# Performance work log

Hardware: AMD Instinct MI355X
Metric: run time of the kernel (lower is better)

The kernel has to match this reference:

```python
import jax, jax.numpy as jnp
import numpy as np

B, S, D_MODEL, H = 2, 2048, 1024, 16
DK = D_MODEL // H
THETA = 10000.0


def setup_inputs() -> dict:
    key = jax.random.key(0)
    ks = jax.random.split(key, 5)
    scale = 0.02  # keep logits in a numerically sane range
    return {
        "x": jax.random.normal(ks[0], (B, S, D_MODEL), jnp.float32),
        "Q_weight": jax.random.normal(ks[1], (D_MODEL, D_MODEL), jnp.float32) * scale,
        "K_weight": jax.random.normal(ks[2], (D_MODEL, D_MODEL), jnp.float32) * scale,
        "V_weight": jax.random.normal(ks[3], (D_MODEL, D_MODEL), jnp.float32) * scale,
        "O_weight": jax.random.normal(ks[4], (D_MODEL, D_MODEL), jnp.float32) * scale,
        "token_positions": jnp.arange(S, dtype=jnp.int32),
    }


def _rope(x, token_positions, theta, d_k):
    # x: [..., seq, d_k]; rotate interleaved even/odd pairs
    inv_freq = 1.0 / theta ** (jnp.arange(0, d_k, 2, dtype=jnp.float32) / d_k)
    ang = token_positions.astype(jnp.float32)[:, None] * inv_freq  # [S, d_k/2]
    cos, sin = jnp.cos(ang), jnp.sin(ang)
    x0, x1 = x[..., 0::2], x[..., 1::2]
    y0 = x0 * cos - x1 * sin
    y1 = x0 * sin + x1 * cos
    return jnp.stack([y0, y1], axis=-1).reshape(x.shape)


def _mhsa(x, Qw, Kw, Vw, Ow, token_positions):
    b, s, d = x.shape
    qw = Qw.reshape(H, DK, d)
    kw = Kw.reshape(H, DK, d)
    vw = Vw.reshape(H, DK, d)
    q = jnp.einsum('hki,bsi->bhsk', qw, x)
    k = jnp.einsum('hki,bsi->bhsk', kw, x)
    v = jnp.einsum('hvi,bsi->bhsv', vw, x)
    q = _rope(q, token_positions, THETA, DK)
    k = _rope(k, token_positions, THETA, DK)
    scores = jnp.einsum('bhnd,bhmd->bhnm', q, k) / jnp.sqrt(jnp.float32(DK))
    causal = jnp.tril(jnp.ones((s, s), dtype=bool))
    scores = jnp.where(causal, scores, -jnp.inf)
    attn = jax.nn.softmax(scores, axis=-1)
    o = jnp.einsum('bhnm,bhmv->bhnv', attn, v)  # [B,H,S,DV]
    o = jnp.transpose(o, (0, 2, 1, 3)).reshape(b, s, H * DK)
    return jnp.einsum('dv,bsv->bsd', Ow, o)


def reference(x, Q_weight, K_weight, V_weight, O_weight, token_positions):
    return _mhsa(x, Q_weight, K_weight, V_weight, O_weight, token_positions)
```

## Files before the change

kernel.cpp:

```cpp
#include <hip/hip_runtime.h>

#define NB 2
#define NS 2048
#define NDM 1024
#define NH 16
#define NDK 64

typedef unsigned int u32;
typedef u32 u32x4 __attribute__((ext_vector_type(4)));
typedef float f32x4 __attribute__((ext_vector_type(4)));
typedef float f32x2 __attribute__((ext_vector_type(2)));
typedef __bf16 bf16x8 __attribute__((ext_vector_type(8)));
typedef __bf16 bf16x4 __attribute__((ext_vector_type(4)));
typedef __bf16 bf16x2 __attribute__((ext_vector_type(2)));

#define QSCALE 0.18033688011112042f
#define EXP2F(x) __builtin_amdgcn_exp2f(x)

__device__ __forceinline__ void gload_lds16(const __bf16* g, __bf16* l) {
    __builtin_amdgcn_global_load_lds(
        (const __attribute__((address_space(1))) unsigned int*)(g),
        (__attribute__((address_space(3))) unsigned int*)(l), 16, 0, 0);
}

__global__ __launch_bounds__(256) void cvt_all(const float* __restrict__ x,
                                               const float* __restrict__ qw,
                                               const float* __restrict__ kw,
                                               const float* __restrict__ vw,
                                               const float* __restrict__ ow,
                                               __bf16* __restrict__ xb,
                                               __bf16* __restrict__ wqkv,
                                               __bf16* __restrict__ owb) {
    const int i = blockIdx.x * 256 + threadIdx.x;
    const float* src;
    __bf16* dst;
    if (i < 1048576) {
        src = x + (size_t)i * 4;
        dst = xb + (size_t)i * 4;
    } else {
        const int j = i - 1048576;
        const int seg = j >> 18;
        const int off = j & 0x3FFFF;
        src = ((seg == 0) ? qw : (seg == 1) ? kw : (seg == 2) ? vw : ow) + (size_t)off * 4;
        dst = ((seg == 3) ? owb : wqkv + (size_t)seg * 1048576) + (size_t)off * 4;
    }
    f32x4 v = *(const f32x4*)src;
    bf16x4 o;
    o[0] = (__bf16)v[0]; o[1] = (__bf16)v[1]; o[2] = (__bf16)v[2]; o[3] = (__bf16)v[3];
    *(bf16x4*)dst = o;
}

__global__ __launch_bounds__(256) void rope_table(const int* __restrict__ tp,
                                                  float* __restrict__ tbl) {
    const int i = blockIdx.x * 256 + threadIdx.x;
    if (i >= NS * 32) return;
    const int s = i >> 5, jj = i & 31;
    const float pos = (float)tp[s];
    const float inv = exp2f(-0.41524101186092f * (float)jj);
    const float ang = pos * inv;
    float sn, cs;
    sincosf(ang, &sn, &cs);
    f32x2 o; o[0] = cs; o[1] = sn;
    *(f32x2*)&tbl[(size_t)i * 2] = o;
}

__global__ __launch_bounds__(512, 2) void gemm256(const __bf16* __restrict__ A,
                                                  const __bf16* __restrict__ Bt,
                                                  __bf16* __restrict__ C,
                                                  __bf16* __restrict__ Vt,
                                                  int K, int lda, int ldb, int ldc, int nbx) {
    __shared__ __bf16 As[2][256 * 64];
    __shared__ __bf16 Bs[2][256 * 64];
    const int tid = threadIdx.x;
    const int lane = tid & 63, w = tid >> 6;
    const int wm = w >> 2, wn = w & 3;
    const int l15 = lane & 15, lg = lane >> 4;
    int bid = blockIdx.x;
    const int cpx = gridDim.x >> 3;
    bid = (bid & 7) * cpx + (bid >> 3);
    const int m0 = (bid / nbx) * 256, n0 = (bid % nbx) * 256;
    const int srow = w * 8 + (lane >> 3);
    const int csw = ((lane & 7) ^ (srow & 7)) * 8;

    f32x4 acc[8][4];
    const f32x4 z = {0.f, 0.f, 0.f, 0.f};
#pragma unroll
    for (int i = 0; i < 8; ++i)
#pragma unroll
        for (int jx = 0; jx < 4; ++jx) acc[i][jx] = z;

    auto stage_pass = [&](int buf, int k0, int ps) {
        const int r = ps * 64 + srow;
        gload_lds16(&A[(size_t)(m0 + r) * lda + k0 + csw], &As[buf][(ps * 64 + w * 8) * 64]);
        gload_lds16(&Bt[(size_t)(n0 + r) * ldb + k0 + csw], &Bs[buf][(ps * 64 + w * 8) * 64]);
    };

#pragma unroll
    for (int ps = 0; ps < 4; ++ps) stage_pass(0, 0, ps);
    int cur = 0;
    for (int k0 = 0; k0 < K; k0 += 64) {
        const bool hasnext = (k0 + 64 < K);
        asm volatile("s_waitcnt vmcnt(0)" ::: "memory");
        __builtin_amdgcn_s_barrier();
        __builtin_amdgcn_sched_barrier(0);
        bf16x8 bfr[4][2];
#pragma unroll
        for (int ph = 0; ph < 4; ++ph) {
            if (ph == 0) {
#pragma unroll
                for (int n = 0; n < 4; ++n)
#pragma unroll
                    for (int kc = 0; kc < 2; ++kc) {
                        const int rb = wn * 64 + n * 16 + l15;
                        bfr[n][kc] = *(const bf16x8*)&Bs[cur][rb * 64 + ((kc * 32 + lg * 8) ^ ((rb & 7) << 3))];
                    }
            }
            bf16x8 a0[2], a1[2];
#pragma unroll
            for (int kc = 0; kc < 2; ++kc) {
                const int ra0 = wm * 128 + (2 * ph) * 16 + l15;
                const int ra1 = wm * 128 + (2 * ph + 1) * 16 + l15;
                a0[kc] = *(const bf16x8*)&As[cur][ra0 * 64 + ((kc * 32 + lg * 8) ^ ((ra0 & 7) << 3))];
                a1[kc] = *(const bf16x8*)&As[cur][ra1 * 64 + ((kc * 32 + lg * 8) ^ ((ra1 & 7) << 3))];
            }
            if (hasnext) stage_pass(cur ^ 1, k0 + 64, ph);
            __builtin_amdgcn_s_barrier();
            asm volatile("s_waitcnt lgkmcnt(0)" ::: "memory");
            __builtin_amdgcn_sched_barrier(0);
            __builtin_amdgcn_s_setprio(1);
#pragma unroll
            for (int n = 0; n < 4; ++n)
#pragma unroll
                for (int kc = 0; kc < 2; ++kc) {
                    acc[2 * ph][n]     = __builtin_amdgcn_mfma_f32_16x16x32_bf16(a0[kc], bfr[n][kc], acc[2 * ph][n], 0, 0, 0);
                    acc[2 * ph + 1][n] = __builtin_amdgcn_mfma_f32_16x16x32_bf16(a1[kc], bfr[n][kc], acc[2 * ph + 1][n], 0, 0, 0);
                }
            __builtin_amdgcn_s_setprio(0);
            __builtin_amdgcn_s_barrier();
            __builtin_amdgcn_sched_barrier(0);
        }
        cur ^= 1;
    }
    if (n0 < 2048) {
#pragma unroll
        for (int mr = 0; mr < 8; ++mr)
#pragma unroll
            for (int n = 0; n < 4; ++n)
#pragma unroll
                for (int j = 0; j < 4; ++j) {
                    const int row = m0 + wm * 128 + mr * 16 + lg * 4 + j;
                    const int col = n0 + wn * 64 + n * 16 + l15;
                    C[(size_t)row * ldc + col] = (__bf16)acc[mr][n][j];
                }
    } else {
#pragma unroll
        for (int mr = 0; mr < 8; ++mr)
#pragma unroll
            for (int n = 0; n < 4; ++n) {
                const int col = (n0 - 2048) + wn * 64 + n * 16 + l15;
                const int h = col >> 6, d = col & 63;
                const int row = m0 + wm * 128 + mr * 16 + lg * 4;
                const int b = row >> 11, s = row & (NS - 1);
                bf16x4 ov;
#pragma unroll
                for (int j = 0; j < 4; ++j) ov[j] = (__bf16)acc[mr][n][j];
                *(bf16x4*)&Vt[((size_t)(b * NH + h) * 64 + d) * NS + s] = ov;
            }
    }
}

template <typename TOUT>
__global__ __launch_bounds__(256) void gemm_bt128(const __bf16* __restrict__ A,
                                                  const __bf16* __restrict__ Bt,
                                                  TOUT* __restrict__ C,
                                                  int K, int lda, int ldb, int ldc) {
    __shared__ __bf16 As[2][128 * 64];
    __shared__ __bf16 Bs[2][128 * 64];
    const int tid = threadIdx.x;
    const int lane = tid & 63, w = tid >> 6;
    const int wr = w >> 1, wc = w & 1;
    const int l15 = lane & 15, lg = lane >> 4;
    const int m0 = blockIdx.y * 128, n0 = blockIdx.x * 128;
    const int crow = lane >> 3;
    const int csw = ((lane & 7) ^ crow) * 8;

    f32x4 acc[4][4];
    const f32x4 z = {0.f, 0.f, 0.f, 0.f};
#pragma unroll
    for (int i = 0; i < 4; ++i)
#pragma unroll
        for (int jx = 0; jx < 4; ++jx) acc[i][jx] = z;

    auto stage = [&](int buf, int k0) {
#pragma unroll
        for (int ch = 0; ch < 4; ++ch) {
            const int cid = w * 4 + ch;
            const int ra = cid * 8 + crow;
            gload_lds16(&A[(size_t)(m0 + ra) * lda + k0 + csw], &As[buf][cid * 512]);
            gload_lds16(&Bt[(size_t)(n0 + ra) * ldb + k0 + csw], &Bs[buf][cid * 512]);
        }
    };

    stage(0, 0);
    int cur = 0;
    for (int k0 = 0; k0 < K; k0 += 64) {
        if (k0 + 64 < K) {
            stage(cur ^ 1, k0 + 64);
            asm volatile("s_waitcnt vmcnt(8)" ::: "memory");
        } else {
            asm volatile("s_waitcnt vmcnt(0)" ::: "memory");
        }
        __builtin_amdgcn_s_barrier();
        __builtin_amdgcn_sched_barrier(0);
#pragma unroll
        for (int kc = 0; kc < 2; ++kc) {
            bf16x8 af[4], bfv[4];
#pragma unroll
            for (int i = 0; i < 4; ++i) {
                const int ra = wr * 64 + i * 16 + l15;
                const int rb = wc * 64 + i * 16 + l15;
                af[i]  = *(const bf16x8*)&As[cur][ra * 64 + ((kc * 32 + lg * 8) ^ ((ra & 7) << 3))];
                bfv[i] = *(const bf16x8*)&Bs[cur][rb * 64 + ((kc * 32 + lg * 8) ^ ((rb & 7) << 3))];
            }
#pragma unroll
            for (int sm = 0; sm < 4; ++sm)
#pragma unroll
                for (int sn = 0; sn < 4; ++sn)
                    acc[sm][sn] = __builtin_amdgcn_mfma_f32_16x16x32_bf16(af[sm], bfv[sn], acc[sm][sn], 0, 0, 0);
        }
        asm volatile("s_waitcnt lgkmcnt(0)" ::: "memory");
        __builtin_amdgcn_s_barrier();
        __builtin_amdgcn_sched_barrier(0);
        cur ^= 1;
    }
#pragma unroll
    for (int sm = 0; sm < 4; ++sm)
#pragma unroll
        for (int sn = 0; sn < 4; ++sn)
#pragma unroll
            for (int j = 0; j < 4; ++j) {
                const int row = m0 + wr * 64 + sm * 16 + lg * 4 + j;
                const int col = n0 + wc * 64 + sn * 16 + l15;
                C[(size_t)row * ldc + col] = (TOUT)acc[sm][sn][j];
            }
}

__global__ __launch_bounds__(512) void rope_kernel(const __bf16* __restrict__ qkv,
                                                   const float* __restrict__ tbl,
                                                   __bf16* __restrict__ Qr,
                                                   __bf16* __restrict__ Kr) {
    const int row = blockIdx.x;
    const int s = row & (NS - 1);
    const int b = row >> 11;
    const int t = threadIdx.x;
    const int h = t >> 5, jj = t & 31;
    f32x2 cssn = *(const f32x2*)&tbl[((size_t)s * 32 + jj) * 2];
    const float cs = cssn[0], sn = cssn[1];
    const __bf16* qp = qkv + (size_t)row * 3072 + h * 64 + 2 * jj;
    bf16x2 qv = *(const bf16x2*)qp;
    bf16x2 kv = *(const bf16x2*)(qp + 1024);
    const float q0 = (float)qv[0], q1 = (float)qv[1];
    const float k0 = (float)kv[0], k1 = (float)kv[1];
    const size_t o = ((size_t)(b * NH + h) * NS + s) * 64 + 2 * jj;
    bf16x2 qo, ko;
    qo[0] = (__bf16)((q0 * cs - q1 * sn) * QSCALE);
    qo[1] = (__bf16)((q0 * sn + q1 * cs) * QSCALE);
    ko[0] = (__bf16)(k0 * cs - k1 * sn); ko[1] = (__bf16)(k0 * sn + k1 * cs);
    *(bf16x2*)&Qr[o] = qo;
    *(bf16x2*)&Kr[o] = ko;
}

__device__ __forceinline__ int kperm(int rt) {
    const int ct = rt >> 4, rr = rt & 15;
    return ((rr >> 2) << 3) + ((ct >> 1) << 5) + ((ct & 1) << 2) + (rr & 3);
}

__global__ __launch_bounds__(256) void attn5(const __bf16* __restrict__ Qr,
                                             const __bf16* __restrict__ Kr,
                                             const __bf16* __restrict__ Vt,
                                             __bf16* __restrict__ O) {
    const int lid = blockIdx.x;
    const int xcd = lid & 7;
    const int g = lid >> 3;
    const int bh = xcd * 4 + (g & 3);
    const int pr = g >> 2;
    const int p = (pr < 8) ? (pr * 2) : (31 - 2 * pr);
    const int b = bh >> 4, h = bh & 15;
    const int tid = threadIdx.x;
    const int w = tid >> 6, lane = tid & 63;
    const int l15 = lane & 15, lg = lane >> 4;
    const __bf16* Qb = Qr + (size_t)bh * NS * 64;
    const __bf16* Kb = Kr + (size_t)bh * NS * 64;
    const __bf16* Vb = Vt + (size_t)bh * 64 * NS;

    __shared__ __bf16 Ks[2][64 * 64];
    __shared__ __bf16 Vs[2][64 * 64];

    const int rbv[2] = {p * 64 + w * 16, (31 - p) * 64 + w * 16};

    bf16x8 qf[2][2];
#pragma unroll
    for (int rs = 0; rs < 2; ++rs)
#pragma unroll
        for (int kc = 0; kc < 2; ++kc)
            qf[rs][kc] = *(const bf16x8*)(Qb + (size_t)(rbv[rs] + l15) * 64 + kc * 32 + lg * 8);

    f32x4 oacc[2][4];
    const f32x4 z = {0.f, 0.f, 0.f, 0.f};
#pragma unroll
    for (int rs = 0; rs < 2; ++rs)
#pragma unroll
        for (int ct = 0; ct < 4; ++ct) oacc[rs][ct] = z;
    float lsum[2] = {0.f, 0.f};

    const int crow = lane >> 3;
    const int cswz = ((lane & 7) ^ crow) * 8;

#pragma unroll
    for (int pp = 0; pp < 2; ++pp) {
        const int ch = w + pp * 4;
        const int rt = ch * 8 + crow;
        gload_lds16(Kb + (size_t)kperm(rt) * 64 + cswz, &Ks[0][ch * 512]);
        gload_lds16(Vb + (size_t)rt * NS + 0 + cswz, &Vs[0][ch * 512]);
    }
    __syncthreads();

    const int nt = 32 - p;
    for (int t = 0; t < nt; ++t) {
        const int cur = t & 1;
        const int kv0 = t << 6;
        if (t + 1 < nt) {
            const int kv1 = kv0 + 64;
#pragma unroll
            for (int pp = 0; pp < 2; ++pp) {
                const int ch = w + pp * 4;
                const int rt = ch * 8 + crow;
                gload_lds16(Kb + (size_t)(kv1 + kperm(rt)) * 64 + cswz, &Ks[cur ^ 1][ch * 512]);
                gload_lds16(Vb + (size_t)rt * NS + kv1 + cswz, &Vs[cur ^ 1][ch * 512]);
            }
        }
        bool act[2];
        act[0] = (kv0 <= rbv[0] + 15);
        act[1] = true;
        f32x4 sc[2][4];
#pragma unroll
        for (int rs = 0; rs < 2; ++rs)
            if (act[rs])
#pragma unroll
                for (int ct = 0; ct < 4; ++ct) sc[rs][ct] = z;
#pragma unroll
        for (int kc = 0; kc < 2; ++kc) {
            bf16x8 kf[4];
#pragma unroll
            for (int ct = 0; ct < 4; ++ct) {
                const int rt = ct * 16 + l15;
                kf[ct] = *(const bf16x8*)&Ks[cur][rt * 64 + ((kc * 32 + lg * 8) ^ ((rt & 7) << 3))];
            }
#pragma unroll
            for (int rs = 0; rs < 2; ++rs)
                if (act[rs])
#pragma unroll
                    for (int ct = 0; ct < 4; ++ct)
                        sc[rs][ct] = __builtin_amdgcn_mfma_f32_16x16x32_bf16(kf[ct], qf[rs][kc], sc[rs][ct], 0, 0, 0);
        }
        bf16x8 pb[2][2];
#pragma unroll
        for (int rs = 0; rs < 2; ++rs) {
            if (!act[rs]) continue;
            const int rbase = rbv[rs];
            const int qrow = rbase + l15;
            const bool needmask = (kv0 + 63 > rbase);
            if (needmask) {
#pragma unroll
                for (int ct = 0; ct < 4; ++ct)
#pragma unroll
                    for (int j = 0; j < 4; ++j) {
                        const int kvg = kv0 + ((ct >> 1) << 5) + lg * 8 + ((ct & 1) << 2) + j;
                        if (kvg > qrow) sc[rs][ct][j] = -1e30f;
                    }
            }
            float ps = 0.f;
#pragma unroll
            for (int ct = 0; ct < 4; ++ct)
#pragma unroll
                for (int j = 0; j < 4; ++j) {
                    const float e = EXP2F(sc[rs][ct][j]);
                    sc[rs][ct][j] = e;
                    ps += e;
                }
            ps += __shfl_xor(ps, 16, 64);
            ps += __shfl_xor(ps, 32, 64);
            lsum[rs] += ps;
#pragma unroll
            for (int kc = 0; kc < 2; ++kc) {
                bf16x8 pk;
                pk[0] = (__bf16)sc[rs][2 * kc][0];     pk[1] = (__bf16)sc[rs][2 * kc][1];
                pk[2] = (__bf16)sc[rs][2 * kc][2];     pk[3] = (__bf16)sc[rs][2 * kc][3];
                pk[4] = (__bf16)sc[rs][2 * kc + 1][0]; pk[5] = (__bf16)sc[rs][2 * kc + 1][1];
                pk[6] = (__bf16)sc[rs][2 * kc + 1][2]; pk[7] = (__bf16)sc[rs][2 * kc + 1][3];
                pb[rs][kc] = pk;
            }
        }
#pragma unroll
        for (int kc = 0; kc < 2; ++kc) {
            bf16x8 vf[4];
#pragma unroll
            for (int ct = 0; ct < 4; ++ct) {
                const int rt = ct * 16 + l15;
                vf[ct] = *(const bf16x8*)&Vs[cur][rt * 64 + ((kc * 32 + lg * 8) ^ ((rt & 7) << 3))];
            }
#pragma unroll
            for (int rs = 0; rs < 2; ++rs) {
                if (!act[rs]) continue;
#pragma unroll
                for (int ct = 0; ct < 4; ++ct)
                    oacc[rs][ct] = __builtin_amdgcn_mfma_f32_16x16x32_bf16(vf[ct], pb[rs][kc], oacc[rs][ct], 0, 0, 0);
            }
        }
        __syncthreads();
    }
#pragma unroll
    for (int rs = 0; rs < 2; ++rs) {
        const float rl = 1.0f / lsum[rs];
        const size_t rowoff = (size_t)(b * NS + rbv[rs] + l15) * NDM + h * 64 + lg * 4;
#pragma unroll
        for (int ct = 0; ct < 4; ++ct) {
            bf16x4 ov;
#pragma unroll
            for (int j = 0; j < 4; ++j) ov[j] = (__bf16)(oacc[rs][ct][j] * rl);
            *(bf16x4*)&O[rowoff + ct * 16] = ov;
        }
    }
}

extern "C" void kernel_launch(void* const* d_in, const int* in_sizes, int n_in,
                              void* d_out, int out_size, void* d_ws, size_t ws_size,
                              hipStream_t stream) {
    const float* x  = (const float*)d_in[0];
    const float* Qw = (const float*)d_in[1];
    const float* Kw = (const float*)d_in[2];
    const float* Vw = (const float*)d_in[3];
    const float* Ow = (const float*)d_in[4];
    const int*   tp = (const int*)d_in[5];
    float* out = (float*)d_out;

    char* ws = (char*)d_ws;
    size_t off = 0;
    auto alloc = [&](size_t bytes) -> void* {
        void* p = ws + off;
        off += (bytes + 255) & ~(size_t)255;
        return p;
    };
    __bf16* xb   = (__bf16*)alloc((size_t)4096 * 1024 * 2);
    __bf16* wqkv = (__bf16*)alloc((size_t)3072 * 1024 * 2);
    __bf16* owb  = (__bf16*)alloc((size_t)1024 * 1024 * 2);
    __bf16* qkv  = (__bf16*)alloc((size_t)4096 * 3072 * 2);
    __bf16* qr   = (__bf16*)alloc((size_t)32 * 2048 * 64 * 2);
    __bf16* kr   = (__bf16*)alloc((size_t)32 * 2048 * 64 * 2);
    __bf16* vt   = (__bf16*)alloc((size_t)32 * 64 * 2048 * 2);
    __bf16* ob   = (__bf16*)alloc((size_t)4096 * 1024 * 2);
    float*  tbl  = (float*)alloc((size_t)NS * 32 * 2 * 4);

    cvt_all<<<8192, 256, 0, stream>>>(x, Qw, Kw, Vw, Ow, xb, wqkv, owb);
    rope_table<<<(NS * 32 + 255) / 256, 256, 0, stream>>>(tp, tbl);

    gemm256<<<192, 512, 0, stream>>>(xb, wqkv, qkv, vt, 1024, 1024, 1024, 3072, 12);
    rope_kernel<<<4096, 512, 0, stream>>>(qkv, tbl, qr, kr);
    attn5<<<dim3(512), 256, 0, stream>>>(qr, kr, vt, ob);
    gemm_bt128<float><<<dim3(1024 / 128, 4096 / 128), 256, 0, stream>>>(
        ob, owb, out, 1024, 1024, 1024, 1024);
}
```

Measured before the change: 119.1 us.

## Use 128-tile QKV GEMM and 2-wave attention with 4 row strips per wave

Replaces the 256x256, 512-thread QKV projection GEMM with a 128x128, 256-thread kernel. The new kernel launches 768 blocks instead of 192, issues the next tile's loads before the MFMA loop, and waits with a partial vmcnt. The attention kernel drops from 4 waves to 2 waves per block, and each wave now owns four 16-row query strips instead of two. This is meant to improve CU fill for the GEMM and to reuse each K/V LDS fragment across more query rows. The cost is higher register pressure in attention and less B-operand reuse per block in the GEMM.

```diff
diff --git a/kernel.cpp b/kernel.cpp
--- a/kernel.cpp
+++ b/kernel.cpp
@@ -64,106 +64,93 @@
     *(f32x2*)&tbl[(size_t)i * 2] = o;
 }
 
-__global__ __launch_bounds__(512, 2) void gemm256(const __bf16* __restrict__ A,
-                                                  const __bf16* __restrict__ Bt,
-                                                  __bf16* __restrict__ C,
-                                                  __bf16* __restrict__ Vt,
-                                                  int K, int lda, int ldb, int ldc, int nbx) {
-    __shared__ __bf16 As[2][256 * 64];
-    __shared__ __bf16 Bs[2][256 * 64];
+__global__ __launch_bounds__(256) void gemm_qkv128(const __bf16* __restrict__ A,
+                                                   const __bf16* __restrict__ Bt,
+                                                   __bf16* __restrict__ C,
+                                                   __bf16* __restrict__ Vt) {
+    __shared__ __bf16 As[2][128 * 64];
+    __shared__ __bf16 Bs[2][128 * 64];
+    const int K = 1024, lda = 1024, ldb = 1024, ldc = 3072;
     const int tid = threadIdx.x;
     const int lane = tid & 63, w = tid >> 6;
-    const int wm = w >> 2, wn = w & 3;
+    const int wr = w >> 1, wc = w & 1;
     const int l15 = lane & 15, lg = lane >> 4;
-    int bid = blockIdx.x;
-    const int cpx = gridDim.x >> 3;
-    bid = (bid & 7) * cpx + (bid >> 3);
-    const int m0 = (bid / nbx) * 256, n0 = (bid % nbx) * 256;
-    const int srow = w * 8 + (lane >> 3);
-    const int csw = ((lane & 7) ^ (srow & 7)) * 8;
-
-    f32x4 acc[8][4];
+    const int m0 = blockIdx.y * 128, n0 = blockIdx.x * 128;
+    const int crow = lane >> 3;
+    const int csw = ((lane & 7) ^ crow) * 8;
+
+    f32x4 acc[4][4];
     const f32x4 z = {0.f, 0.f, 0.f, 0.f};
 #pragma unroll
-    for (int i = 0; i < 8; ++i)
+    for (int i = 0; i < 4; ++i)
 #pragma unroll
         for (int jx = 0; jx < 4; ++jx) acc[i][jx] = z;
 
-    auto stage_pass = [&](int buf, int k0, int ps) {
-        const int r = ps * 64 + srow;
-        gload_lds16(&A[(size_t)(m0 + r) * lda + k0 + csw], &As[buf][(ps * 64 + w * 8) * 64]);
-        gload_lds16(&Bt[(size_t)(n0 + r) * ldb + k0 + csw], &Bs[buf][(ps * 64 + w * 8) * 64]);
+    auto stage = [&](int buf, int k0) {
+#pragma unroll
+        for (int ch = 0; ch < 4; ++ch) {
+            const int cid = w * 4 + ch;
+            const int ra = cid * 8 + crow;
+            gload_lds16(&A[(size_t)(m0 + ra) * lda + k0 + csw], &As[buf][cid * 512]);
+            gload_lds16(&Bt[(size_t)(n0 + ra) * ldb + k0 + csw], &Bs[buf][cid * 512]);
+        }
     };
 
-#pragma unroll
-    for (int ps = 0; ps < 4; ++ps) stage_pass(0, 0, ps);
+    stage(0, 0);
     int cur = 0;
     for (int k0 = 0; k0 < K; k0 += 64) {
-        const bool hasnext = (k0 + 64 < K);
-        asm volatile("s_waitcnt vmcnt(0)" ::: "memory");
+        if (k0 + 64 < K) {
+            stage(cur ^ 1, k0 + 64);
+            asm volatile("s_waitcnt vmcnt(8)" ::: "memory");
+        } else {
+            asm volatile("s_waitcnt vmcnt(0)" ::: "memory");
+        }
         __builtin_amdgcn_s_barrier();
         __builtin_amdgcn_sched_barrier(0);
-        bf16x8 bfr[4][2];
-#pragma unroll
-        for (int ph = 0; ph < 4; ++ph) {
-            if (ph == 0) {
-#pragma unroll
-                for (int n = 0; n < 4; ++n)
-#pragma unroll
-                    for (int kc = 0; kc < 2; ++kc) {
-                        const int rb = wn * 64 + n * 16 + l15;
-                        bfr[n][kc] = *(const bf16x8*)&Bs[cur][rb * 64 + ((kc * 32 + lg * 8) ^ ((rb & 7) << 3))];
-                    }
-            }
-            bf16x8 a0[2], a1[2];
-#pragma unroll
-            for (int kc = 0; kc < 2; ++kc) {
-                const int ra0 = wm * 128 + (2 * ph) * 16 + l15;
-                const int ra1 = wm * 128 + (2 * ph + 1) * 16 + l15;
-                a0[kc] = *(const bf16x8*)&As[cur][ra0 * 64 + ((kc * 32 + lg * 8) ^ ((ra0 & 7) << 3))];
-                a1[kc] = *(const bf16x8*)&As[cur][ra1 * 64 + ((kc * 32 + lg * 8) ^ ((ra1 & 7) << 3))];
-            }
-            if (hasnext) stage_pass(cur ^ 1, k0 + 64, ph);
-            __builtin_amdgcn_s_barrier();
-            asm volatile("s_waitcnt lgkmcnt(0)" ::: "memory");
-            __builtin_amdgcn_sched_barrier(0);
-            __builtin_amdgcn_s_setprio(1);
-#pragma unroll
-            for (int n = 0; n < 4; ++n)
-#pragma unroll
-                for (int kc = 0; kc < 2; ++kc) {
-                    acc[2 * ph][n]     = __builtin_amdgcn_mfma_f32_16x16x32_bf16(a0[kc], bfr[n][kc], acc[2 * ph][n], 0, 0, 0);
-                    acc[2 * ph + 1][n] = __builtin_amdgcn_mfma_f32_16x16x32_bf16(a1[kc], bfr[n][kc], acc[2 * ph + 1][n], 0, 0, 0);
-                }
-            __builtin_amdgcn_s_setprio(0);
-            __builtin_amdgcn_s_barrier();
-            __builtin_amdgcn_sched_barrier(0);
-        }
+#pragma unroll
+        for (int kc = 0; kc < 2; ++kc) {
+            bf16x8 af[4], bfv[4];
+#pragma unroll
+            for (int i = 0; i < 4; ++i) {
+                const int ra = wr * 64 + i * 16 + l15;
+                const int rb = wc * 64 + i * 16 + l15;
+                af[i]  = *(const bf16x8*)&As[cur][ra * 64 + ((kc * 32 + lg * 8) ^ ((ra & 7) << 3))];
+                bfv[i] = *(const bf16x8*)&Bs[cur][rb * 64 + ((kc * 32 + lg * 8) ^ ((rb & 7) << 3))];
+            }
+#pragma unroll
+            for (int sm = 0; sm < 4; ++sm)
+#pragma unroll
+                for (int sn = 0; sn < 4; ++sn)
+                    acc[sm][sn] = __builtin_amdgcn_mfma_f32_16x16x32_bf16(af[sm], bfv[sn], acc[sm][sn], 0, 0, 0);
+        }
+        asm volatile("s_waitcnt lgkmcnt(0)" ::: "memory");
+        __builtin_amdgcn_s_barrier();
+        __builtin_amdgcn_sched_barrier(0);
         cur ^= 1;
     }
     if (n0 < 2048) {
 #pragma unroll
-        for (int mr = 0; mr < 8; ++mr)
-#pragma unroll
-            for (int n = 0; n < 4; ++n)
+        for (int sm = 0; sm < 4; ++sm)
+#pragma unroll
+            for (int sn = 0; sn < 4; ++sn)
 #pragma unroll
                 for (int j = 0; j < 4; ++j) {
-                    const int row = m0 + wm * 128 + mr * 16 + lg * 4 + j;
-                    const int col = n0 + wn * 64 + n * 16 + l15;
-                    C[(size_t)row * ldc + col] = (__bf16)acc[mr][n][j];
+                    const int row = m0 + wr * 64 + sm * 16 + lg * 4 + j;
+                    const int col = n0 + wc * 64 + sn * 16 + l15;
+                    C[(size_t)row * ldc + col] = (__bf16)acc[sm][sn][j];
                 }
     } else {
 #pragma unroll
-        for (int mr = 0; mr < 8; ++mr)
-#pragma unroll
-            for (int n = 0; n < 4; ++n) {
-                const int col = (n0 - 2048) + wn * 64 + n * 16 + l15;
+        for (int sm = 0; sm < 4; ++sm)
+#pragma unroll
+            for (int sn = 0; sn < 4; ++sn) {
+                const int col = (n0 - 2048) + wc * 64 + sn * 16 + l15;
                 const int h = col >> 6, d = col & 63;
-                const int row = m0 + wm * 128 + mr * 16 + lg * 4;
+                const int row = m0 + wr * 64 + sm * 16 + lg * 4;
                 const int b = row >> 11, s = row & (NS - 1);
                 bf16x4 ov;
 #pragma unroll
-                for (int j = 0; j < 4; ++j) ov[j] = (__bf16)acc[mr][n][j];
+                for (int j = 0; j < 4; ++j) ov[j] = (__bf16)acc[sm][sn][j];
                 *(bf16x4*)&Vt[((size_t)(b * NH + h) * 64 + d) * NS + s] = ov;
             }
     }
@@ -275,7 +262,7 @@
     return ((rr >> 2) << 3) + ((ct >> 1) << 5) + ((ct & 1) << 2) + (rr & 3);
 }
 
-__global__ __launch_bounds__(256) void attn5(const __bf16* __restrict__ Qr,
+__global__ __launch_bounds__(128) void attn7(const __bf16* __restrict__ Qr,
                                              const __bf16* __restrict__ Kr,
                                              const __bf16* __restrict__ Vt,
                                              __bf16* __restrict__ O) {
@@ -296,29 +283,30 @@
     __shared__ __bf16 Ks[2][64 * 64];
     __shared__ __bf16 Vs[2][64 * 64];
 
-    const int rbv[2] = {p * 64 + w * 16, (31 - p) * 64 + w * 16};
-
-    bf16x8 qf[2][2];
-#pragma unroll
-    for (int rs = 0; rs < 2; ++rs)
+    const int rbv[4] = {p * 64 + w * 32, p * 64 + w * 32 + 16,
+                        (31 - p) * 64 + w * 32, (31 - p) * 64 + w * 32 + 16};
+
+    bf16x8 qf[4][2];
+#pragma unroll
+    for (int rs = 0; rs < 4; ++rs)
 #pragma unroll
         for (int kc = 0; kc < 2; ++kc)
             qf[rs][kc] = *(const bf16x8*)(Qb + (size_t)(rbv[rs] + l15) * 64 + kc * 32 + lg * 8);
 
-    f32x4 oacc[2][4];
+    f32x4 oacc[4][4];
     const f32x4 z = {0.f, 0.f, 0.f, 0.f};
 #pragma unroll
-    for (int rs = 0; rs < 2; ++rs)
+    for (int rs = 0; rs < 4; ++rs)
 #pragma unroll
         for (int ct = 0; ct < 4; ++ct) oacc[rs][ct] = z;
-    float lsum[2] = {0.f, 0.f};
+    float lsum[4] = {0.f, 0.f, 0.f, 0.f};
 
     const int crow = lane >> 3;
     const int cswz = ((lane & 7) ^ crow) * 8;
 
 #pragma unroll
-    for (int pp = 0; pp < 2; ++pp) {
-        const int ch = w + pp * 4;
+    for (int pp = 0; pp < 4; ++pp) {
+        const int ch = w + pp * 2;
         const int rt = ch * 8 + crow;
         gload_lds16(Kb + (size_t)kperm(rt) * 64 + cswz, &Ks[0][ch * 512]);
         gload_lds16(Vb + (size_t)rt * NS + 0 + cswz, &Vs[0][ch * 512]);
@@ -332,19 +320,19 @@
         if (t + 1 < nt) {
             const int kv1 = kv0 + 64;
 #pragma unroll
-            for (int pp = 0; pp < 2; ++pp) {
-                const int ch = w + pp * 4;
+            for (int pp = 0; pp < 4; ++pp) {
+                const int ch = w + pp * 2;
                 const int rt = ch * 8 + crow;
                 gload_lds16(Kb + (size_t)(kv1 + kperm(rt)) * 64 + cswz, &Ks[cur ^ 1][ch * 512]);
                 gload_lds16(Vb + (size_t)rt * NS + kv1 + cswz, &Vs[cur ^ 1][ch * 512]);
             }
         }
-        bool act[2];
-        act[0] = (kv0 <= rbv[0] + 15);
-        act[1] = true;
-        f32x4 sc[2][4];
-#pragma unroll
-        for (int rs = 0; rs < 2; ++rs)
+        bool act[4];
+#pragma unroll
+        for (int rs = 0; rs < 4; ++rs) act[rs] = (kv0 <= rbv[rs] + 15);
+        f32x4 sc[4][4];
+#pragma unroll
+        for (int rs = 0; rs < 4; ++rs)
             if (act[rs])
 #pragma unroll
                 for (int ct = 0; ct < 4; ++ct) sc[rs][ct] = z;
@@ -357,15 +345,15 @@
                 kf[ct] = *(const bf16x8*)&Ks[cur][rt * 64 + ((kc * 32 + lg * 8) ^ ((rt & 7) << 3))];
             }
 #pragma unroll
-            for (int rs = 0; rs < 2; ++rs)
+            for (int rs = 0; rs < 4; ++rs)
                 if (act[rs])
 #pragma unroll
                     for (int ct = 0; ct < 4; ++ct)
                         sc[rs][ct] = __builtin_amdgcn_mfma_f32_16x16x32_bf16(kf[ct], qf[rs][kc], sc[rs][ct], 0, 0, 0);
         }
-        bf16x8 pb[2][2];
-#pragma unroll
-        for (int rs = 0; rs < 2; ++rs) {
+        bf16x8 pb[4][2];
+#pragma unroll
+        for (int rs = 0; rs < 4; ++rs) {
             if (!act[rs]) continue;
             const int rbase = rbv[rs];
             const int qrow = rbase + l15;
@@ -410,7 +398,7 @@
                 vf[ct] = *(const bf16x8*)&Vs[cur][rt * 64 + ((kc * 32 + lg * 8) ^ ((rt & 7) << 3))];
             }
 #pragma unroll
-            for (int rs = 0; rs < 2; ++rs) {
+            for (int rs = 0; rs < 4; ++rs) {
                 if (!act[rs]) continue;
 #pragma unroll
                 for (int ct = 0; ct < 4; ++ct)
@@ -420,7 +408,7 @@
         __syncthreads();
     }
 #pragma unroll
-    for (int rs = 0; rs < 2; ++rs) {
+    for (int rs = 0; rs < 4; ++rs) {
         const float rl = 1.0f / lsum[rs];
         const size_t rowoff = (size_t)(b * NS + rbv[rs] + l15) * NDM + h * 64 + lg * 4;
 #pragma unroll
@@ -464,9 +452,9 @@
     cvt_all<<<8192, 256, 0, stream>>>(x, Qw, Kw, Vw, Ow, xb, wqkv, owb);
     rope_table<<<(NS * 32 + 255) / 256, 256, 0, stream>>>(tp, tbl);
 
-    gemm256<<<192, 512, 0, stream>>>(xb, wqkv, qkv, vt, 1024, 1024, 1024, 3072, 12);
+    gemm_qkv128<<<dim3(3072 / 128, 4096 / 128), 256, 0, stream>>>(xb, wqkv, qkv, vt);
     rope_kernel<<<4096, 512, 0, stream>>>(qkv, tbl, qr, kr);
-    attn5<<<dim3(512), 256, 0, stream>>>(qr, kr, vt, ob);
+    attn7<<<dim3(512), 128, 0, stream>>>(qr, kr, vt, ob);
     gemm_bt128<float><<<dim3(1024 / 128, 4096 / 128), 256, 0, stream>>>(
         ob, owb, out, 1024, 1024, 1024, 1024);
 }
```

New measurement: 142.1 us. 19.3% more time.
